# Kernel optimization log

Hardware: AMD Instinct MI355X
Metric: run time of the kernel (lower is better)

## Reference

```python
import jax, jax.numpy as jnp
import numpy as np

N_EMBD = 1024
N_HEAD = 16
B, T, T_MEM = 4, 1024, 1024


def setup_inputs() -> dict:
    key = jax.random.key(0)
    ks = jax.random.split(key, 11)
    s = 1.0 / np.sqrt(N_EMBD)
    inp = {
        "q_in": jax.random.normal(ks[0], (B, T, N_EMBD), jnp.float32),
        "k_in": jax.random.normal(ks[1], (B, T_MEM, N_EMBD), jnp.float32),
        "v_in": jax.random.normal(ks[2], (B, T_MEM, N_EMBD), jnp.float32),
        "Wq": jax.random.normal(ks[3], (N_EMBD, N_EMBD), jnp.float32) * s,
        "bq": jnp.zeros((N_EMBD,), jnp.float32),
        "Wk": jax.random.normal(ks[4], (N_EMBD, N_EMBD), jnp.float32) * s,
        "bk": jnp.zeros((N_EMBD,), jnp.float32),
        "Wv": jax.random.normal(ks[5], (N_EMBD, N_EMBD), jnp.float32) * s,
        "bv": jnp.zeros((N_EMBD,), jnp.float32),
        "Wo": jax.random.normal(ks[6], (N_EMBD, N_EMBD), jnp.float32) * s,
        "bo": jnp.zeros((N_EMBD,), jnp.float32),
    }
    return inp


def reference(q_in, k_in, v_in, Wq, bq, Wk, bk, Wv, bv, Wo, bo):
    b, t, c = q_in.shape
    t_mem = k_in.shape[1]
    h = N_HEAD
    hs = c // h
    # torch Linear: x @ W.T + b
    q = (q_in @ Wq.T + bq).reshape(b, t, h, hs).transpose(0, 2, 1, 3)      # [b,h,t,hs]
    k = (k_in @ Wk.T + bk).reshape(b, t_mem, h, hs).transpose(0, 2, 1, 3)  # [b,h,tm,hs]
    v = (v_in @ Wv.T + bv).reshape(b, t_mem, h, hs).transpose(0, 2, 1, 3)
    att = jnp.einsum('bhtd,bhsd->bhts', q, k) * (1.0 / np.sqrt(hs))        # [b,h,t,tm]
    att = jax.nn.softmax(att, axis=-1)
    # dropout is identity (pdrop=0 / eval mode)
    y = jnp.einsum('bhts,bhsd->bhtd', att, v)                              # [b,h,t,hs]
    y = y.transpose(0, 2, 1, 3).reshape(b, t, c)
    y = y @ Wo.T + bo
    attention = att.mean(axis=1)                                           # [b,t,tm]
    return (y, attention)
```

## Files before the change

### kernel.cpp

```cpp
#include <hip/hip_runtime.h>

typedef unsigned short ushort_t;
typedef __attribute__((ext_vector_type(8))) __bf16 bf16x8;
typedef __attribute__((ext_vector_type(4))) float f32x4;

#define GLD(src, lds) __builtin_amdgcn_global_load_lds( \
    (const __attribute__((address_space(1))) void*)(src), \
    (__attribute__((address_space(3))) void*)(lds), 16, 0, 0)

#if __has_builtin(__builtin_amdgcn_exp2f)
#define EXP2(x) __builtin_amdgcn_exp2f(x)
#else
#define EXP2(x) __expf((x) * 0.69314718f)
#endif
#define QK_SCALE 0.18033688f

static __device__ __forceinline__ f32x4 mfma16(bf16x8 a, bf16x8 b, f32x4 c){
  return __builtin_amdgcn_mfma_f32_16x16x32_bf16(a, b, c, 0, 0, 0);
}
static __device__ __forceinline__ ushort_t f2bf(float f){
  unsigned u = __float_as_uint(f);
  return (ushort_t)((u + 0x7FFFu + ((u >> 16) & 1u)) >> 16);
}

template<int ROWS>
static __device__ __forceinline__ void stage64(const ushort_t* __restrict__ g, size_t rstride,
                                               ushort_t* lds, int tid){
#pragma unroll
  for (int r = 0; r < ROWS/32; ++r){
    int li = r*256 + tid;
    int row = li >> 3, ch = li & 7;
    GLD(g + (size_t)row*rstride + ((ch ^ (row & 7)) << 3),
        (char*)lds + (r*256 + (tid >> 6)*64)*16);
  }
}
static __device__ __forceinline__ bf16x8 frag64(const ushort_t* lds, int row, int ch){
  return *(const bf16x8*)((const char*)lds + row*128 + ((ch ^ (row & 7)) << 4));
}

static __device__ __forceinline__ void stage32(const ushort_t* __restrict__ g, size_t rstride,
                                               ushort_t* lds, int tid){
#pragma unroll
  for (int r = 0; r < 2; ++r){
    int li = r*256 + tid;
    int row = li >> 2, ch = li & 3;
    GLD(g + (size_t)row*rstride + ((ch ^ ((row >> 1) & 3)) << 3),
        (char*)lds + (r*256 + (tid >> 6)*64)*16);
  }
}
static __device__ __forceinline__ bf16x8 frag32(const ushort_t* lds, int row, int ch){
  return *(const bf16x8*)((const char*)lds + row*64 + ((ch ^ ((row >> 1) & 3)) << 4));
}

__global__ __launch_bounds__(256) void cast_all(const float* __restrict__ q,
    const float* __restrict__ k, const float* __restrict__ v,
    const float* __restrict__ wq, const float* __restrict__ wk,
    const float* __restrict__ wv, const float* __restrict__ wo,
    char* __restrict__ ws)
{
  const size_t MB = 1024*1024;
  int i = blockIdx.x*256 + threadIdx.x;
  const float* src; ushort_t* dst; int j;
  if (i < 1048576){ src = q; dst = (ushort_t*)(ws); j = i; }
  else if (i < 2097152){ src = k; dst = (ushort_t*)(ws + 8*MB); j = i - 1048576; }
  else if (i < 3145728){ src = v; dst = (ushort_t*)(ws + 16*MB); j = i - 2097152; }
  else {
    int t = i - 3145728, w = t >> 18; j = t & 262143;
    src = w==0 ? wq : w==1 ? wk : w==2 ? wv : wo;
    dst = (ushort_t*)(ws + (24 + 2*(size_t)w)*MB);
  }
  float4 x = ((const float4*)src)[j];
  ushort4 o;
  o.x = f2bf(x.x); o.y = f2bf(x.y); o.z = f2bf(x.z); o.w = f2bf(x.w);
  ((ushort4*)dst)[j] = o;
}

static __device__ __forceinline__ void gemm_body(const ushort_t* __restrict__ A,
    const ushort_t* __restrict__ B, const float* __restrict__ bias,
    void* __restrict__ Cout, int bx, int mode, char* smem)
{
  constexpr int K = 1024;
  const int tid = threadIdx.x, lane = tid & 63, wv = tid >> 6;
  const int fr = lane & 15, fq = lane >> 4;
  const int wr = wv >> 1, wc = wv & 1;
  const int brow0 = ((bx & 7) * 4 + ((bx >> 3) & 3)) * 128;
  const int bcol0 = (bx >> 5) * 128;

  const f32x4 zero = {0.f, 0.f, 0.f, 0.f};
  f32x4 acc[4][4];
#pragma unroll
  for (int m = 0; m < 4; ++m)
#pragma unroll
    for (int n = 0; n < 4; ++n) acc[m][n] = zero;

  const ushort_t* Abase = A + (size_t)brow0*K;
  const ushort_t* Bbase = B + (size_t)bcol0*K;

  stage32(Abase,      K, (ushort_t*)(smem),             tid);
  stage32(Bbase,      K, (ushort_t*)(smem + 24576),     tid);
  stage32(Abase + 32, K, (ushort_t*)(smem + 8192),      tid);
  stage32(Bbase + 32, K, (ushort_t*)(smem + 24576 + 8192), tid);
  asm volatile("s_waitcnt vmcnt(4)" ::: "memory");
  __builtin_amdgcn_s_barrier();

  int rd = 0, wrb = 2;
  for (int kt = 0; kt < 32; ++kt){
    if (kt < 30){
      stage32(Abase + (kt+2)*32, K, (ushort_t*)(smem + wrb*8192),         tid);
      stage32(Bbase + (kt+2)*32, K, (ushort_t*)(smem + 24576 + wrb*8192), tid);
    }
    const ushort_t* Ac = (const ushort_t*)(smem + rd*8192);
    const ushort_t* Bc = (const ushort_t*)(smem + 24576 + rd*8192);
    bf16x8 af[4], bfg[4];
#pragma unroll
    for (int m = 0; m < 4; ++m) af[m]  = frag32(Ac, wr*64 + m*16 + fr, fq);
#pragma unroll
    for (int n = 0; n < 4; ++n) bfg[n] = frag32(Bc, wc*64 + n*16 + fr, fq);
    __builtin_amdgcn_s_setprio(1);
#pragma unroll
    for (int m = 0; m < 4; ++m)
#pragma unroll
      for (int n = 0; n < 4; ++n)
        acc[m][n] = mfma16(af[m], bfg[n], acc[m][n]);
    __builtin_amdgcn_s_setprio(0);
    __builtin_amdgcn_sched_barrier(0);
    if (kt < 30) asm volatile("s_waitcnt vmcnt(4)" ::: "memory");
    else         asm volatile("s_waitcnt vmcnt(0)" ::: "memory");
    __builtin_amdgcn_s_barrier();
    rd  = (rd  == 2) ? 0 : rd  + 1;
    wrb = (wrb == 2) ? 0 : wrb + 1;
  }

#pragma unroll
  for (int n = 0; n < 4; ++n){
    const int colg = bcol0 + wc*64 + n*16 + fr;
    const float bv = bias[colg];
#pragma unroll
    for (int m = 0; m < 4; ++m){
      const int rowg0 = brow0 + wr*64 + m*16 + fq*4;
      if (mode == 1){
        int b = rowg0 >> 10, t = rowg0 & 1023, h = colg >> 6, d = colg & 63;
        ushort4 o;
        o.x = f2bf(acc[m][n][0] + bv); o.y = f2bf(acc[m][n][1] + bv);
        o.z = f2bf(acc[m][n][2] + bv); o.w = f2bf(acc[m][n][3] + bv);
        *(ushort4*)((ushort_t*)Cout + (((size_t)(b*16 + h))*64 + d)*1024 + t) = o;
      } else {
#pragma unroll
        for (int r = 0; r < 4; ++r){
          const int rowg = rowg0 + r;
          float val = acc[m][n][r] + bv;
          if (mode == 0){
            int b = rowg >> 10, t = rowg & 1023, h = colg >> 6, d = colg & 63;
            ((ushort_t*)Cout)[(((size_t)(b*16 + h))*1024 + t)*64 + d] = f2bf(val);
          } else {
            ((float*)Cout)[(size_t)rowg*1024 + colg] = val;
          }
        }
      }
    }
  }
}

__global__ __launch_bounds__(256) void gemm_qkv(const ushort_t* qb, const ushort_t* kb,
    const ushort_t* vb, const ushort_t* wqb, const ushort_t* wkb, const ushort_t* wvb,
    const float* bq, const float* bk, const float* bv,
    ushort_t* Qm, ushort_t* Km, ushort_t* Vtm)
{
  __shared__ char smem[49152];
  int id = blockIdx.x >> 8, bx = blockIdx.x & 255;
  const ushort_t* A = id==0 ? qb : id==1 ? kb : vb;
  const ushort_t* B = id==0 ? wqb : id==1 ? wkb : wvb;
  const float* bias = id==0 ? bq : id==1 ? bk : bv;
  void* C = id==0 ? (void*)Qm : id==1 ? (void*)Km : (void*)Vtm;
  gemm_body(A, B, bias, C, bx, id==2 ? 1 : 0, smem);
}

static __device__ __forceinline__ void attmean_body(const ushort_t* __restrict__ Q,
    const ushort_t* __restrict__ Kmat, const float* __restrict__ Lrow,
    float* __restrict__ attOut, int nb, char* smem)
{
  ushort_t* Qs0 = (ushort_t*)smem;
  ushort_t* Qs1 = (ushort_t*)(smem + 8192);
  ushort_t* Ks0 = (ushort_t*)(smem + 16384);
  ushort_t* Ks1 = (ushort_t*)(smem + 32768);
  const int tid = threadIdx.x, lane = tid & 63, wv = tid >> 6;
  const int fr = lane & 15, fq = lane >> 4;
  const int c_ = nb & 7, k_ = nb >> 3;
  const int b = c_ >> 1;
  const int rem = (c_ & 1)*64 + k_;
  const int t0 = (rem >> 3) * 64, s0 = (rem & 7) * 128;

  const f32x4 zero = {0.f, 0.f, 0.f, 0.f};
  f32x4 acc[2][4];
#pragma unroll
  for (int c = 0; c < 2; ++c)
#pragma unroll
    for (int n = 0; n < 4; ++n) acc[c][n] = zero;

  stage64<64>(Q + ((size_t)(b*16)*1024 + t0)*64, 64, Qs0, tid);
  stage64<128>(Kmat + ((size_t)(b*16)*1024 + s0)*64, 64, Ks0, tid);
  __syncthreads();

  for (int h = 0; h < 16; ++h){
    const int cur = h & 1;
    ushort_t* Qc = cur ? Qs1 : Qs0;
    ushort_t* Kc = cur ? Ks1 : Ks0;
    ushort_t* Qn = cur ? Qs0 : Qs1;
    ushort_t* Kn = cur ? Ks0 : Ks1;
    if (h < 15){
      stage64<64>(Q + ((size_t)(b*16 + h+1)*1024 + t0)*64, 64, Qn, tid);
      stage64<128>(Kmat + ((size_t)(b*16 + h+1)*1024 + s0)*64, 64, Kn, tid);
    }
    const int bh = b*16 + h;
    bf16x8 qf0 = frag64(Qc, wv*16 + fr, fq);
    bf16x8 qf1 = frag64(Qc, wv*16 + fr, 4 + fq);
    const float il = 1.f / Lrow[bh*1024 + t0 + wv*16 + fr];
#pragma unroll
    for (int c = 0; c < 2; ++c){
      f32x4 sfr[4];
      __builtin_amdgcn_s_setprio(1);
#pragma unroll
      for (int n = 0; n < 4; ++n){
        f32x4 s0v = mfma16(frag64(Kc, c*64 + n*16 + fr, fq), qf0, zero);
        sfr[n] = mfma16(frag64(Kc, c*64 + n*16 + fr, 4 + fq), qf1, s0v);
      }
      __builtin_amdgcn_s_setprio(0);
#pragma unroll
      for (int n = 0; n < 4; ++n)
#pragma unroll
        for (int r = 0; r < 4; ++r)
          acc[c][n][r] += EXP2(sfr[n][r] * QK_SCALE) * il;
    }
    __syncthreads();
  }

  const float s16 = 1.f/16.f;
#pragma unroll
  for (int c = 0; c < 2; ++c)
#pragma unroll
    for (int n = 0; n < 4; ++n){
      f32x4 v = acc[c][n];
      v[0] *= s16; v[1] *= s16; v[2] *= s16; v[3] *= s16;
      size_t idx = ((size_t)b << 20) + (size_t)(t0 + wv*16 + fr)*1024 + s0 + c*64 + n*16 + fq*4;
      *(f32x4*)(attOut + idx) = v;
    }
}

__global__ __launch_bounds__(256) void fused_tail(const ushort_t* __restrict__ Yws,
    const ushort_t* __restrict__ Wob, const float* __restrict__ bo, float* __restrict__ y_out,
    const ushort_t* __restrict__ Qm, const ushort_t* __restrict__ Km,
    const float* __restrict__ Lrow, float* __restrict__ att_out)
{
  __shared__ char smem[49152];
  const int bx = blockIdx.x;
  if (bx < 256) gemm_body(Yws, Wob, bo, y_out, bx, 2, smem);
  else          attmean_body(Qm, Km, Lrow, att_out, bx - 256, smem);
}

__global__ __launch_bounds__(256, 2) void flash_kernel(const ushort_t* __restrict__ Q,
                                                       const ushort_t* __restrict__ Kmat,
                                                       const ushort_t* __restrict__ Vt,
                                                       ushort_t* __restrict__ Yws,
                                                       float* __restrict__ Lrow)
{
  __shared__ ushort_t Ks[2][64][64];
  __shared__ ushort_t Vts[2][64][64];
  __shared__ ushort_t Ps[4][32][64];
  const int tid = threadIdx.x, lane = tid & 63, wv = tid >> 6;
  const int fr = lane & 15, fq = lane >> 4;
  const int nb = blockIdx.x;
  const int bh = (nb & 7)*8 + (nb >> 6);
  const int t0 = ((nb >> 3) & 7) * 128;

  stage64<128>(Q + ((size_t)bh*1024 + t0)*64, 64, &Ps[0][0][0], tid);
  stage64<64>(Kmat + (size_t)bh*1024*64, 64, &Ks[0][0][0], tid);
  stage64<64>(Vt + (size_t)bh*64*1024, 1024, &Vts[0][0][0], tid);
  __syncthreads();
  bf16x8 aQ[2][2];
#pragma unroll
  for (int mt = 0; mt < 2; ++mt)
#pragma unroll
    for (int h = 0; h < 2; ++h)
      aQ[mt][h] = frag64(&Ps[0][0][0], wv*32 + mt*16 + fr, h*4 + fq);
  __syncthreads();

  bf16x8 ones;
#pragma unroll
  for (int i = 0; i < 8; ++i) ones[i] = (__bf16)1.0f;

  const f32x4 zero = {0.f, 0.f, 0.f, 0.f};
  f32x4 o_acc[2][4], l_acc[2];
#pragma unroll
  for (int mt = 0; mt < 2; ++mt){
    l_acc[mt] = zero;
#pragma unroll
    for (int n = 0; n < 4; ++n) o_acc[mt][n] = zero;
  }
  char* myP = (char*)&Ps[wv][0][0];

  for (int sc = 0; sc < 16; ++sc){
    const int cur = sc & 1;
    if (sc < 15){
      stage64<64>(Kmat + ((size_t)bh*1024 + (sc+1)*64)*64, 64, &Ks[cur^1][0][0], tid);
      stage64<64>(Vt + (size_t)bh*64*1024 + (sc+1)*64, 1024, &Vts[cur^1][0][0], tid);
    }
    bf16x8 kf[4][2];
#pragma unroll
    for (int n = 0; n < 4; ++n){
      kf[n][0] = frag64(&Ks[cur][0][0], n*16 + fr, fq);
      kf[n][1] = frag64(&Ks[cur][0][0], n*16 + fr, 4 + fq);
    }
    f32x4 sfr[2][4];
    __builtin_amdgcn_s_setprio(1);
#pragma unroll
    for (int mt = 0; mt < 2; ++mt)
#pragma unroll
      for (int n = 0; n < 4; ++n){
        f32x4 s0 = mfma16(kf[n][0], aQ[mt][0], zero);
        sfr[mt][n] = mfma16(kf[n][1], aQ[mt][1], s0);
      }
    __builtin_amdgcn_s_setprio(0);
#pragma unroll
    for (int mt = 0; mt < 2; ++mt){
#pragma unroll
      for (int n = 0; n < 4; ++n){
        float p0 = EXP2(sfr[mt][n][0] * QK_SCALE);
        float p1 = EXP2(sfr[mt][n][1] * QK_SCALE);
        float p2 = EXP2(sfr[mt][n][2] * QK_SCALE);
        float p3 = EXP2(sfr[mt][n][3] * QK_SCALE);
        uint2 w;
        w.x = (unsigned)f2bf(p0) | ((unsigned)f2bf(p1) << 16);
        w.y = (unsigned)f2bf(p2) | ((unsigned)f2bf(p3) << 16);
        *(uint2*)(myP + mt*2048 + fr*128 + (((n*4 + fq) ^ (fr & 14)) << 3)) = w;
      }
    }
    asm volatile("s_waitcnt lgkmcnt(0)" ::: "memory");
    __builtin_amdgcn_sched_barrier(0);
    __builtin_amdgcn_s_setprio(1);
#pragma unroll
    for (int ks = 0; ks < 2; ++ks){
      bf16x8 pa[2];
#pragma unroll
      for (int mt = 0; mt < 2; ++mt){
        uint4 u = *(const uint4*)(myP + mt*2048 + fr*128 + (((ks*8 + fq*2) ^ (fr & 14)) << 3));
        pa[mt] = __builtin_bit_cast(bf16x8, u);
      }
#pragma unroll
      for (int n = 0; n < 4; ++n){
        bf16x8 vf = frag64(&Vts[cur][0][0], n*16 + fr, ks*4 + fq);
#pragma unroll
        for (int mt = 0; mt < 2; ++mt)
          o_acc[mt][n] = mfma16(pa[mt], vf, o_acc[mt][n]);
      }
#pragma unroll
      for (int mt = 0; mt < 2; ++mt)
        l_acc[mt] = mfma16(pa[mt], ones, l_acc[mt]);
    }
    __builtin_amdgcn_s_setprio(0);
    __syncthreads();
  }

  const int b = bh >> 4, h = bh & 15;
#pragma unroll
  for (int mt = 0; mt < 2; ++mt){
    float inv[4];
#pragma unroll
    for (int r = 0; r < 4; ++r) inv[r] = 1.f / l_acc[mt][r];
#pragma unroll
    for (int n = 0; n < 4; ++n)
#pragma unroll
      for (int r = 0; r < 4; ++r){
        size_t row = (size_t)b*1024 + t0 + wv*32 + mt*16 + fq*4 + r;
        Yws[row*1024 + h*64 + n*16 + fr] = f2bf(o_acc[mt][n][r] * inv[r]);
      }
  }
  if (fr == 0){
#pragma unroll
    for (int mt = 0; mt < 2; ++mt)
#pragma unroll
      for (int r = 0; r < 4; ++r)
        Lrow[bh*1024 + t0 + wv*32 + mt*16 + fq*4 + r] = l_acc[mt][r];
  }
}

extern "C" void kernel_launch(void* const* d_in, const int* in_sizes, int n_in,
                              void* d_out, int out_size, void* d_ws, size_t ws_size,
                              hipStream_t stream)
{
  const float* q_in = (const float*)d_in[0];
  const float* k_in = (const float*)d_in[1];
  const float* v_in = (const float*)d_in[2];
  const float* Wq   = (const float*)d_in[3];
  const float* bq   = (const float*)d_in[4];
  const float* Wk   = (const float*)d_in[5];
  const float* bk   = (const float*)d_in[6];
  const float* Wv   = (const float*)d_in[7];
  const float* bv   = (const float*)d_in[8];
  const float* Wo   = (const float*)d_in[9];
  const float* bo   = (const float*)d_in[10];

  float* y_out   = (float*)d_out;
  float* att_out = y_out + (size_t)4*1024*1024;

  char* ws = (char*)d_ws;
  const size_t MB = 1024*1024;
  ushort_t* qb   = (ushort_t*)(ws + 0);
  ushort_t* kb   = (ushort_t*)(ws + 8*MB);
  ushort_t* vb   = (ushort_t*)(ws + 16*MB);
  ushort_t* wqb  = (ushort_t*)(ws + 24*MB);
  ushort_t* wkb  = (ushort_t*)(ws + 26*MB);
  ushort_t* wvb  = (ushort_t*)(ws + 28*MB);
  ushort_t* wob  = (ushort_t*)(ws + 30*MB);
  ushort_t* Qm   = (ushort_t*)(ws + 32*MB);
  ushort_t* Km   = (ushort_t*)(ws + 40*MB);
  ushort_t* Vtm  = (ushort_t*)(ws + 48*MB);
  ushort_t* Yws  = (ushort_t*)(ws + 56*MB);
  float*    Lrow = (float*)(ws + 64*MB);

  cast_all<<<16384, 256, 0, stream>>>(q_in, k_in, v_in, Wq, Wk, Wv, Wo, ws);

  gemm_qkv<<<768, 256, 0, stream>>>(qb, kb, vb, wqb, wkb, wvb, bq, bk, bv, Qm, Km, Vtm);

  flash_kernel<<<512, 256, 0, stream>>>(Qm, Km, Vtm, Yws, Lrow);

  fused_tail<<<768, 256, 0, stream>>>(Yws, wob, bo, y_out, Qm, Km, Lrow, att_out);
}
```

Before: 128.2 us.

## Fuse fp32-to-bf16 activation cast into QKV projection GEMM loads

Removes the separate cast of q/k/v activations to bf16 and instead has the QKV GEMM stage fp32 activation tiles directly into LDS, converting them to bf16 while building MFMA fragments. Weights are still cast by a smaller kernel. This removes one full read and write of the 48 MB of activations. In exchange the GEMM streams twice the bytes of A per tile, uses a simpler double-buffered pipeline with full __syncthreads instead of the previous triple-buffered vmcnt schedule, and converts in registers inside the inner loop.

Result: slower. 173.0 us (+35.0%).

```diff
diff --git a/kernel.cpp b/kernel.cpp
--- a/kernel.cpp
+++ b/kernel.cpp
@@ -52,27 +52,122 @@
   return *(const bf16x8*)((const char*)lds + row*64 + ((ch ^ ((row >> 1) & 3)) << 4));
 }
 
-__global__ __launch_bounds__(256) void cast_all(const float* __restrict__ q,
-    const float* __restrict__ k, const float* __restrict__ v,
-    const float* __restrict__ wq, const float* __restrict__ wk,
-    const float* __restrict__ wv, const float* __restrict__ wo,
-    char* __restrict__ ws)
+static __device__ __forceinline__ void stageA(const float* __restrict__ g, size_t rstride,
+                                              float* lds, int tid){
+#pragma unroll
+  for (int r = 0; r < 4; ++r){
+    int li = r*256 + tid;
+    int row = li >> 3, ch = li & 7;
+    GLD(g + (size_t)row*rstride + ((ch ^ (row & 7)) << 2),
+        (char*)lds + (r*256 + (tid >> 6)*64)*16);
+  }
+}
+static __device__ __forceinline__ bf16x8 fragA(const float* lds, int row, int fq){
+  const char* base = (const char*)lds + row*128;
+  f32x4 a = *(const f32x4*)(base + (((2*fq)     ^ (row & 7)) << 4));
+  f32x4 b = *(const f32x4*)(base + (((2*fq + 1) ^ (row & 7)) << 4));
+  bf16x8 o;
+  o[0] = (__bf16)a[0]; o[1] = (__bf16)a[1]; o[2] = (__bf16)a[2]; o[3] = (__bf16)a[3];
+  o[4] = (__bf16)b[0]; o[5] = (__bf16)b[1]; o[6] = (__bf16)b[2]; o[7] = (__bf16)b[3];
+  return o;
+}
+
+__global__ __launch_bounds__(256) void cast_w(const float* __restrict__ wq,
+    const float* __restrict__ wk, const float* __restrict__ wv,
+    const float* __restrict__ wo, char* __restrict__ ws)
 {
   const size_t MB = 1024*1024;
   int i = blockIdx.x*256 + threadIdx.x;
-  const float* src; ushort_t* dst; int j;
-  if (i < 1048576){ src = q; dst = (ushort_t*)(ws); j = i; }
-  else if (i < 2097152){ src = k; dst = (ushort_t*)(ws + 8*MB); j = i - 1048576; }
-  else if (i < 3145728){ src = v; dst = (ushort_t*)(ws + 16*MB); j = i - 2097152; }
-  else {
-    int t = i - 3145728, w = t >> 18; j = t & 262143;
-    src = w==0 ? wq : w==1 ? wk : w==2 ? wv : wo;
-    dst = (ushort_t*)(ws + (24 + 2*(size_t)w)*MB);
-  }
+  int w = i >> 18, j = i & 262143;
+  const float* src = w==0 ? wq : w==1 ? wk : w==2 ? wv : wo;
+  ushort_t* dst = (ushort_t*)(ws + (24 + 2*(size_t)w)*MB);
   float4 x = ((const float4*)src)[j];
   ushort4 o;
   o.x = f2bf(x.x); o.y = f2bf(x.y); o.z = f2bf(x.z); o.w = f2bf(x.w);
   ((ushort4*)dst)[j] = o;
+}
+
+template<int MODE>
+static __device__ __forceinline__ void gemm_f32_body(const float* __restrict__ A,
+    const ushort_t* __restrict__ B, const float* __restrict__ bias,
+    void* __restrict__ Cout, int bx)
+{
+  constexpr int K = 1024;
+  __shared__ float    Asf[2][128][32];
+  __shared__ ushort_t Bs [2][128][32];
+  const int tid = threadIdx.x, lane = tid & 63, wv = tid >> 6;
+  const int fr = lane & 15, fq = lane >> 4;
+  const int wr = wv >> 1, wc = wv & 1;
+  const int brow0 = ((bx & 7) * 4 + ((bx >> 3) & 3)) * 128;
+  const int bcol0 = (bx >> 5) * 128;
+
+  const f32x4 zero = {0.f, 0.f, 0.f, 0.f};
+  f32x4 acc[4][4];
+#pragma unroll
+  for (int m = 0; m < 4; ++m)
+#pragma unroll
+    for (int n = 0; n < 4; ++n) acc[m][n] = zero;
+
+  stageA(A + (size_t)brow0*K, K, &Asf[0][0][0], tid);
+  stage32(B + (size_t)bcol0*K, K, &Bs[0][0][0], tid);
+  __syncthreads();
+
+  for (int kt = 0; kt < K/32; ++kt){
+    const int cur = kt & 1;
+    if (kt < K/32 - 1){
+      stageA(A + (size_t)brow0*K + (kt+1)*32, K, &Asf[cur^1][0][0], tid);
+      stage32(B + (size_t)bcol0*K + (kt+1)*32, K, &Bs[cur^1][0][0], tid);
+    }
+    bf16x8 af[4], bfg[4];
+#pragma unroll
+    for (int m = 0; m < 4; ++m) af[m]  = fragA(&Asf[cur][0][0], wr*64 + m*16 + fr, fq);
+#pragma unroll
+    for (int n = 0; n < 4; ++n) bfg[n] = frag32(&Bs[cur][0][0], wc*64 + n*16 + fr, fq);
+    __builtin_amdgcn_s_setprio(1);
+#pragma unroll
+    for (int m = 0; m < 4; ++m)
+#pragma unroll
+      for (int n = 0; n < 4; ++n)
+        acc[m][n] = mfma16(af[m], bfg[n], acc[m][n]);
+    __builtin_amdgcn_s_setprio(0);
+    __syncthreads();
+  }
+
+#pragma unroll
+  for (int n = 0; n < 4; ++n){
+    const int colg = bcol0 + wc*64 + n*16 + fr;
+    const float bv = bias[colg];
+#pragma unroll
+    for (int m = 0; m < 4; ++m){
+      const int rowg0 = brow0 + wr*64 + m*16 + fq*4;
+      if (MODE == 1){
+        int b = rowg0 >> 10, t = rowg0 & 1023, h = colg >> 6, d = colg & 63;
+        ushort4 o;
+        o.x = f2bf(acc[m][n][0] + bv); o.y = f2bf(acc[m][n][1] + bv);
+        o.z = f2bf(acc[m][n][2] + bv); o.w = f2bf(acc[m][n][3] + bv);
+        *(ushort4*)((ushort_t*)Cout + (((size_t)(b*16 + h))*64 + d)*1024 + t) = o;
+      } else {
+#pragma unroll
+        for (int r = 0; r < 4; ++r){
+          const int rowg = rowg0 + r;
+          float val = acc[m][n][r] + bv;
+          int b = rowg >> 10, t = rowg & 1023, h = colg >> 6, d = colg & 63;
+          ((ushort_t*)Cout)[(((size_t)(b*16 + h))*1024 + t)*64 + d] = f2bf(val);
+        }
+      }
+    }
+  }
+}
+
+__global__ __launch_bounds__(256) void gemm_qkv(const float* q, const float* k,
+    const float* v, const ushort_t* wqb, const ushort_t* wkb, const ushort_t* wvb,
+    const float* bq, const float* bk, const float* bv,
+    ushort_t* Qm, ushort_t* Km, ushort_t* Vtm)
+{
+  int id = blockIdx.x >> 8, bx = blockIdx.x & 255;
+  if (id == 0)      gemm_f32_body<0>(q, wqb, bq, Qm,  bx);
+  else if (id == 1) gemm_f32_body<0>(k, wkb, bk, Km,  bx);
+  else              gemm_f32_body<1>(v, wvb, bv, Vtm, bx);
 }
 
 static __device__ __forceinline__ void gemm_body(const ushort_t* __restrict__ A,
@@ -138,41 +233,15 @@
 #pragma unroll
     for (int m = 0; m < 4; ++m){
       const int rowg0 = brow0 + wr*64 + m*16 + fq*4;
-      if (mode == 1){
-        int b = rowg0 >> 10, t = rowg0 & 1023, h = colg >> 6, d = colg & 63;
-        ushort4 o;
-        o.x = f2bf(acc[m][n][0] + bv); o.y = f2bf(acc[m][n][1] + bv);
-        o.z = f2bf(acc[m][n][2] + bv); o.w = f2bf(acc[m][n][3] + bv);
-        *(ushort4*)((ushort_t*)Cout + (((size_t)(b*16 + h))*64 + d)*1024 + t) = o;
-      } else {
-#pragma unroll
-        for (int r = 0; r < 4; ++r){
-          const int rowg = rowg0 + r;
-          float val = acc[m][n][r] + bv;
-          if (mode == 0){
-            int b = rowg >> 10, t = rowg & 1023, h = colg >> 6, d = colg & 63;
-            ((ushort_t*)Cout)[(((size_t)(b*16 + h))*1024 + t)*64 + d] = f2bf(val);
-          } else {
-            ((float*)Cout)[(size_t)rowg*1024 + colg] = val;
-          }
-        }
-      }
-    }
-  }
-}
-
-__global__ __launch_bounds__(256) void gemm_qkv(const ushort_t* qb, const ushort_t* kb,
-    const ushort_t* vb, const ushort_t* wqb, const ushort_t* wkb, const ushort_t* wvb,
-    const float* bq, const float* bk, const float* bv,
-    ushort_t* Qm, ushort_t* Km, ushort_t* Vtm)
-{
-  __shared__ char smem[49152];
-  int id = blockIdx.x >> 8, bx = blockIdx.x & 255;
-  const ushort_t* A = id==0 ? qb : id==1 ? kb : vb;
-  const ushort_t* B = id==0 ? wqb : id==1 ? wkb : wvb;
-  const float* bias = id==0 ? bq : id==1 ? bk : bv;
-  void* C = id==0 ? (void*)Qm : id==1 ? (void*)Km : (void*)Vtm;
-  gemm_body(A, B, bias, C, bx, id==2 ? 1 : 0, smem);
+#pragma unroll
+      for (int r = 0; r < 4; ++r){
+        const int rowg = rowg0 + r;
+        float val = acc[m][n][r] + bv;
+        ((float*)Cout)[(size_t)rowg*1024 + colg] = val;
+      }
+    }
+  }
+  (void)mode;
 }
 
 static __device__ __forceinline__ void attmean_body(const ushort_t* __restrict__ Q,
@@ -404,9 +473,6 @@
 
   char* ws = (char*)d_ws;
   const size_t MB = 1024*1024;
-  ushort_t* qb   = (ushort_t*)(ws + 0);
-  ushort_t* kb   = (ushort_t*)(ws + 8*MB);
-  ushort_t* vb   = (ushort_t*)(ws + 16*MB);
   ushort_t* wqb  = (ushort_t*)(ws + 24*MB);
   ushort_t* wkb  = (ushort_t*)(ws + 26*MB);
   ushort_t* wvb  = (ushort_t*)(ws + 28*MB);
@@ -417,9 +483,10 @@
   ushort_t* Yws  = (ushort_t*)(ws + 56*MB);
   float*    Lrow = (float*)(ws + 64*MB);
 
-  cast_all<<<16384, 256, 0, stream>>>(q_in, k_in, v_in, Wq, Wk, Wv, Wo, ws);
-
-  gemm_qkv<<<768, 256, 0, stream>>>(qb, kb, vb, wqb, wkb, wvb, bq, bk, bv, Qm, Km, Vtm);
+  cast_w<<<4096, 256, 0, stream>>>(Wq, Wk, Wv, Wo, ws);
+
+  gemm_qkv<<<768, 256, 0, stream>>>(q_in, k_in, v_in, wqb, wkb, wvb,
+                                    bq, bk, bv, Qm, Km, Vtm);
 
   flash_kernel<<<512, 256, 0, stream>>>(Qm, Km, Vtm, Yws, Lrow);
 
```
